# Optimization experiments

Hardware: AMD Instinct MI355X
Metric: run time of the kernel (lower is better)

## Reference

```python
import jax, jax.numpy as jnp
import numpy as np

INPUT_DIM = 1024
HIDDEN_DIM = 1024


def setup_inputs() -> dict:
    key = jax.random.key(0)
    ks = jax.random.split(key, 7)
    s = 1.0 / np.sqrt(INPUT_DIM)
    x = jax.random.normal(ks[0], (4, 2048, INPUT_DIM), dtype=jnp.float32)
    Wq = jax.random.uniform(ks[1], (INPUT_DIM, HIDDEN_DIM), minval=-s, maxval=s, dtype=jnp.float32)
    bq = jax.random.uniform(ks[2], (HIDDEN_DIM,), minval=-s, maxval=s, dtype=jnp.float32)
    Wk = jax.random.uniform(ks[3], (INPUT_DIM, HIDDEN_DIM), minval=-s, maxval=s, dtype=jnp.float32)
    bk = jax.random.uniform(ks[4], (HIDDEN_DIM,), minval=-s, maxval=s, dtype=jnp.float32)
    Wv = jax.random.uniform(ks[5], (INPUT_DIM, HIDDEN_DIM), minval=-s, maxval=s, dtype=jnp.float32)
    bv = jax.random.uniform(ks[6], (HIDDEN_DIM,), minval=-s, maxval=s, dtype=jnp.float32)
    return {"x": x, "Wq": Wq, "bq": bq, "Wk": Wk, "bk": bk, "Wv": Wv, "bv": bv}


def reference(x, Wq, bq, Wk, bk, Wv, bv):
    # Q, K, V: [B, S, H]
    Q = jnp.einsum('bsd,dh->bsh', x, Wq) + bq
    K = jnp.einsum('bsd,dh->bsh', x, Wk) + bk
    V = jnp.einsum('bsd,dh->bsh', x, Wv) + bv
    scale = 1.0 / jnp.sqrt(jnp.array(Q.shape[-1], dtype=Q.dtype))
    scores = jnp.einsum('bqh,bkh->bqk', Q, K) * scale  # [B, S, S]
    attn = jax.nn.softmax(scores, axis=-1)
    return jnp.einsum('bqk,bkh->bqh', attn, V)
```

## Files before the change

### kernel.cpp

```cpp
#include <hip/hip_runtime.h>
#include <hip/hip_bf16.h>
#include <stdint.h>

typedef unsigned short u16;
typedef __attribute__((ext_vector_type(8))) short short8;
typedef __attribute__((ext_vector_type(4))) float floatx4;

#define BATCH 4
#define SEQ   2048
#define DIM   1024

__device__ inline u16 f2bf(float f) {
  union { float f; uint32_t u; } v; v.f = f;
  uint32_t r = v.u + 0x7fffu + ((v.u >> 16) & 1u);
  return (u16)(r >> 16);
}

__device__ inline uint32_t f2bf2(float lo, float hi) {
  __hip_bfloat162 h = __float22bfloat162_rn(float2{lo, hi});
  union { __hip_bfloat162 h; uint32_t u; } v; v.h = h;
  return v.u;
}

__device__ inline void gload_lds16(const u16* g, u16* l) {
  __builtin_amdgcn_global_load_lds((const __attribute__((address_space(1))) uint32_t*)g,
                                   (__attribute__((address_space(3))) uint32_t*)l,
                                   16, 0, 0);
}

__global__ __launch_bounds__(256) void cvt_x(const float* __restrict__ in,
                                             u16* __restrict__ out,
                                             float* __restrict__ lsum) {
  size_t i = ((size_t)blockIdx.x * 256 + threadIdx.x) * 4;
  float4 v = *(const float4*)(in + i);
  uint2 o;
  o.x = f2bf2(v.x, v.y);
  o.y = f2bf2(v.z, v.w);
  *(uint2*)(out + i) = o;
  if (blockIdx.x < 8) {
    float4 z = {0.f, 0.f, 0.f, 0.f};
    *(float4*)(lsum + (size_t)blockIdx.x * 1024 + threadIdx.x * 4) = z;
  }
}

__global__ __launch_bounds__(256) void transpose_w(const float* __restrict__ Wq,
                                                   const float* __restrict__ Wk,
                                                   const float* __restrict__ Wv,
                                                   const float* __restrict__ bq,
                                                   const float* __restrict__ bk,
                                                   const float* __restrict__ bv,
                                                   u16* __restrict__ out,
                                                   float* __restrict__ bias) {
  const float* W = (blockIdx.z == 0) ? Wq : (blockIdx.z == 1) ? Wk : Wv;
  u16* o = out + (size_t)blockIdx.z * (1u << 20);
  if (blockIdx.x == 0 && blockIdx.y == 0) {
    const float* bsrc = (blockIdx.z == 0) ? bq : (blockIdx.z == 1) ? bk : bv;
    float4 b4 = *(const float4*)(bsrc + threadIdx.x * 4);
    *(float4*)(bias + blockIdx.z * 1024 + threadIdx.x * 4) = b4;
  }
  __shared__ u16 tile[32][33];
  int c0 = blockIdx.x * 32, r0 = blockIdx.y * 32;
  int tx = threadIdx.x & 31, ty = threadIdx.x >> 5;
#pragma unroll
  for (int p = 0; p < 4; ++p)
    tile[p * 8 + ty][tx] = f2bf(W[(size_t)(r0 + p * 8 + ty) * DIM + c0 + tx]);
  __syncthreads();
#pragma unroll
  for (int p = 0; p < 4; ++p)
    o[(size_t)(c0 + p * 8 + ty) * DIM + r0 + tx] = tile[tx][p * 8 + ty];
}

template <int EPI, int SWIZ, int TM>
__global__ __launch_bounds__(256, (TM == 256) ? 2 : 3)
void gemm_bt(const u16* __restrict__ A, const u16* __restrict__ Bt,
             void* __restrict__ Cv, const float* __restrict__ bias,
             float* __restrict__ lsum, int M, int N, int K,
             size_t sA, size_t sB, size_t sC) {
  constexpr int MI = TM / 32;
  constexpr int AS = TM / 64;
  __shared__ u16 ldsA[TM * 64];
  __shared__ u16 ldsB[128 * 64];
  const int lane = threadIdx.x & 63;
  const int wave = threadIdx.x >> 6;

  int mt, nt;
  if (SWIZ == 0) {
    mt = blockIdx.x; nt = blockIdx.y;
  } else if (SWIZ == 1) {
    const int lin = blockIdx.x;
    const int c = lin & 7, j = lin >> 3;
    mt = 4 * (c & 3) + (j & 3);
    nt = 8 * (c >> 2) + (j >> 2);
  } else if (SWIZ == 2) {
    const int lin = blockIdx.x;
    const int c = lin & 7, j = lin >> 3;
    mt = 4 * (c >> 1) + (j & 3);
    nt = 4 * (c & 1) + (j >> 2);
  } else if (SWIZ == 3) {
    nt = blockIdx.x; mt = blockIdx.y;
  } else {
    const int lin = blockIdx.x;
    const int c = lin & 7, j = lin >> 3;
    mt = 4 * (c & 1) + (j & 3);
    nt = 4 * (c >> 1) + (j >> 2);
  }

  const u16* Ab = A + sA * blockIdx.z + (size_t)mt * TM * K;
  const u16* Bb = Bt + sB * blockIdx.z + (size_t)nt * 128 * K;

  const int sr = lane >> 2;
  const int sc = (lane & 3) * 8;
  const u16* gA0 = Ab + (size_t)(wave * (TM / 4) + sr) * K + sc;
  const u16* gB0 = Bb + (size_t)(wave * 32 + sr) * K + sc;
  u16* lA0 = ldsA + wave * (TM / 4) * 32;
  u16* lB0 = ldsB + wave * 1024;
  constexpr int SLA = TM * 32;
  constexpr int SLB = 4096;

  const int wm = (wave >> 1) * (TM / 2);
  const int wn = (wave & 1) * 64;
  const int fr = lane & 15;
  const int fk = (lane >> 4) * 8;
  const u16* la = ldsA + (wm + fr) * 32 + fk;
  const u16* lb = ldsB + (wn + fr) * 32 + fk;

  floatx4 acc[MI][4] = {};

  for (int kt = 0; kt < K; kt += 64) {
    __syncthreads();
#pragma unroll
    for (int i = 0; i < AS; ++i) {
      gload_lds16(gA0 + kt + (size_t)(16 * i) * K, lA0 + i * 512);
      gload_lds16(gA0 + kt + 32 + (size_t)(16 * i) * K, lA0 + SLA + i * 512);
    }
#pragma unroll
    for (int i = 0; i < 2; ++i) {
      gload_lds16(gB0 + kt + (size_t)(16 * i) * K, lB0 + i * 512);
      gload_lds16(gB0 + kt + 32 + (size_t)(16 * i) * K, lB0 + SLB + i * 512);
    }
    __syncthreads();
#pragma unroll
    for (int ks = 0; ks < 2; ++ks) {
      short8 a[MI], b[4];
#pragma unroll
      for (int i = 0; i < MI; ++i)
        a[i] = *(const short8*)(la + ks * SLA + i * 512);
#pragma unroll
      for (int i = 0; i < 4; ++i)
        b[i] = *(const short8*)(lb + ks * SLB + i * 512);
#pragma unroll
      for (int mi = 0; mi < MI; ++mi)
#pragma unroll
        for (int ni = 0; ni < 4; ++ni)
          acc[mi][ni] = __builtin_amdgcn_mfma_f32_16x16x32_bf16(a[mi], b[ni], acc[mi][ni], 0, 0, 0);
    }
  }

  const int er = (lane >> 4) * 4;
  const int ec = lane & 15;
  const int r0 = mt * TM + wm;
  const int c0 = nt * 128 + wn;

  if (EPI == 0) {
    u16* C = (u16*)Cv + sC * blockIdx.z;
    const float* bz = bias + blockIdx.z * 1024;
    const float zs = (blockIdx.z == 0) ? 0.03125f : 1.0f;
#pragma unroll
    for (int mi = 0; mi < MI; ++mi)
#pragma unroll
      for (int ni = 0; ni < 4; ++ni) {
        const int col = c0 + ni * 16 + ec;
        const float bb = bz[col];
        const int row = r0 + mi * 16 + er;
        const uint32_t p0 = f2bf2((acc[mi][ni][0] + bb) * zs, (acc[mi][ni][1] + bb) * zs);
        const uint32_t p1 = f2bf2((acc[mi][ni][2] + bb) * zs, (acc[mi][ni][3] + bb) * zs);
        C[(size_t)(row + 0) * N + col] = (u16)p0;
        C[(size_t)(row + 1) * N + col] = (u16)(p0 >> 16);
        C[(size_t)(row + 2) * N + col] = (u16)p1;
        C[(size_t)(row + 3) * N + col] = (u16)(p1 >> 16);
      }
  } else if (EPI == 1) {
    u16* C = (u16*)Cv + sC * blockIdx.z;
    float* lz = lsum + blockIdx.z * 2048;
#pragma unroll
    for (int mi = 0; mi < MI; ++mi) {
      float rs[4] = {0.f, 0.f, 0.f, 0.f};
#pragma unroll
      for (int ni = 0; ni < 4; ++ni) {
        const int col = c0 + ni * 16 + ec;
        const int row = r0 + mi * 16 + er;
        float e[4];
#pragma unroll
        for (int r = 0; r < 4; ++r) {
          e[r] = exp2f(acc[mi][ni][r] * 1.44269504088896340736f);
          rs[r] += e[r];
        }
        const uint32_t p0 = f2bf2(e[0], e[1]);
        const uint32_t p1 = f2bf2(e[2], e[3]);
        C[(size_t)(row + 0) * N + col] = (u16)p0;
        C[(size_t)(row + 1) * N + col] = (u16)(p0 >> 16);
        C[(size_t)(row + 2) * N + col] = (u16)p1;
        C[(size_t)(row + 3) * N + col] = (u16)(p1 >> 16);
      }
#pragma unroll
      for (int o = 1; o < 16; o <<= 1)
#pragma unroll
        for (int r = 0; r < 4; ++r) rs[r] += __shfl_xor(rs[r], o);
      if ((lane & 15) == 0) {
#pragma unroll
        for (int r = 0; r < 4; ++r)
          atomicAdd(&lz[r0 + mi * 16 + er + r], rs[r]);
      }
    }
  } else if (EPI == 2) {
    float* C = (float*)Cv + sC * blockIdx.z;
    const float* lz = lsum + blockIdx.z * 2048;
#pragma unroll
    for (int mi = 0; mi < MI; ++mi) {
      float inv[4];
#pragma unroll
      for (int r = 0; r < 4; ++r) inv[r] = 1.0f / lz[r0 + mi * 16 + er + r];
#pragma unroll
      for (int ni = 0; ni < 4; ++ni) {
        const int col = c0 + ni * 16 + ec;
#pragma unroll
        for (int r = 0; r < 4; ++r) {
          const int row = r0 + mi * 16 + er + r;
          C[(size_t)row * N + col] = acc[mi][ni][r] * inv[r];
        }
      }
    }
  } else {
    u16* C = (u16*)Cv;
    const float* bz = bias + 2 * 1024;
#pragma unroll
    for (int mi = 0; mi < MI; ++mi) {
      float bb[4];
#pragma unroll
      for (int r = 0; r < 4; ++r) bb[r] = bz[r0 + mi * 16 + er + r];
#pragma unroll
      for (int ni = 0; ni < 4; ++ni) {
        const int col = c0 + ni * 16 + ec;
        const size_t base = (size_t)(col >> 11) * (1u << 21) + (col & 2047);
        const int row = r0 + mi * 16 + er;
        const uint32_t p0 = f2bf2(acc[mi][ni][0] + bb[0], acc[mi][ni][1] + bb[1]);
        const uint32_t p1 = f2bf2(acc[mi][ni][2] + bb[2], acc[mi][ni][3] + bb[3]);
        C[base + (size_t)(row + 0) * 2048] = (u16)p0;
        C[base + (size_t)(row + 1) * 2048] = (u16)(p0 >> 16);
        C[base + (size_t)(row + 2) * 2048] = (u16)p1;
        C[base + (size_t)(row + 3) * 2048] = (u16)(p1 >> 16);
      }
    }
  }
}

extern "C" void kernel_launch(void* const* d_in, const int* in_sizes, int n_in,
                              void* d_out, int out_size, void* d_ws, size_t ws_size,
                              hipStream_t stream) {
  const float* x  = (const float*)d_in[0];
  const float* Wq = (const float*)d_in[1];
  const float* bq = (const float*)d_in[2];
  const float* Wk = (const float*)d_in[3];
  const float* bk = (const float*)d_in[4];
  const float* Wv = (const float*)d_in[5];
  const float* bv = (const float*)d_in[6];
  float* out = (float*)d_out;

  char* ws = (char*)d_ws;
  const size_t MB = 1ull << 20;
  u16* Q    = (u16*)(ws + 0 * MB);
  u16* Kb   = (u16*)(ws + 16 * MB);
  u16* Vt   = (u16*)(ws + 48 * MB);
  u16* Xb   = (u16*)(ws + 64 * MB);
  u16* Wt   = (u16*)(ws + 80 * MB);
  float* bias = (float*)(ws + 86 * MB);
  float* lsum = (float*)(ws + 87 * MB);
  u16* P    = (u16*)(ws + 88 * MB);
  (void)Kb; (void)ws_size; (void)in_sizes; (void)n_in; (void)out_size;

  cvt_x<<<8192, 256, 0, stream>>>(x, Xb, lsum);
  transpose_w<<<dim3(32, 32, 3), 256, 0, stream>>>(Wq, Wk, Wv, bq, bk, bv, Wt, bias);
  gemm_bt<0, 0, 256><<<dim3(32, 8, 2), 256, 0, stream>>>(
      Xb, Wt, Q, bias, nullptr, 8192, 1024, 1024,
      (size_t)0, (size_t)(1u << 20), (size_t)(8u << 20));
  gemm_bt<3, 3, 128><<<dim3(64, 8, 1), 256, 0, stream>>>(
      Wt + 2 * (1u << 20), Xb, Vt, bias, nullptr, 1024, 8192, 1024,
      (size_t)0, (size_t)0, (size_t)0);
  gemm_bt<1, 4, 256><<<dim3(128, 1, 4), 256, 0, stream>>>(
      Q, Kb, P, nullptr, lsum, 2048, 2048, 1024,
      (size_t)2097152, (size_t)2097152, (size_t)4194304);
  gemm_bt<2, 2, 128><<<dim3(128, 1, 4), 256, 0, stream>>>(
      P, Vt, out, nullptr, lsum, 2048, 1024, 2048,
      (size_t)4194304, (size_t)2097152, (size_t)2097152);
}
```

Baseline: 238.0 us.

## Merge prep kernels and fuse Q/K/V projections into one launch

The x-conversion and weight-transpose kernels become a single prep kernel that dispatches on block index. The Q/K projection (256-row tiles) and the V projection (transposed output) are folded into one qkv_fused kernel with 128x128 tiles and a z dimension of 3. This removes two kernel launches and lets the V GEMM overlap with the Q/K GEMMs in one grid. In exchange, Q/K now use smaller tiles, which means more global reloads per output, and the V epilogue keeps its scattered transposed stores.

```diff
diff --git a/kernel.cpp b/kernel.cpp
--- a/kernel.cpp
+++ b/kernel.cpp
@@ -28,38 +28,44 @@
                                    16, 0, 0);
 }
 
-__global__ __launch_bounds__(256) void cvt_x(const float* __restrict__ in,
-                                             u16* __restrict__ out,
-                                             float* __restrict__ lsum) {
-  size_t i = ((size_t)blockIdx.x * 256 + threadIdx.x) * 4;
-  float4 v = *(const float4*)(in + i);
-  uint2 o;
-  o.x = f2bf2(v.x, v.y);
-  o.y = f2bf2(v.z, v.w);
-  *(uint2*)(out + i) = o;
-  if (blockIdx.x < 8) {
-    float4 z = {0.f, 0.f, 0.f, 0.f};
-    *(float4*)(lsum + (size_t)blockIdx.x * 1024 + threadIdx.x * 4) = z;
-  }
-}
-
-__global__ __launch_bounds__(256) void transpose_w(const float* __restrict__ Wq,
-                                                   const float* __restrict__ Wk,
-                                                   const float* __restrict__ Wv,
-                                                   const float* __restrict__ bq,
-                                                   const float* __restrict__ bk,
-                                                   const float* __restrict__ bv,
-                                                   u16* __restrict__ out,
-                                                   float* __restrict__ bias) {
-  const float* W = (blockIdx.z == 0) ? Wq : (blockIdx.z == 1) ? Wk : Wv;
-  u16* o = out + (size_t)blockIdx.z * (1u << 20);
-  if (blockIdx.x == 0 && blockIdx.y == 0) {
-    const float* bsrc = (blockIdx.z == 0) ? bq : (blockIdx.z == 1) ? bk : bv;
+__global__ __launch_bounds__(256) void prep(const float* __restrict__ x,
+                                            const float* __restrict__ Wq,
+                                            const float* __restrict__ Wk,
+                                            const float* __restrict__ Wv,
+                                            const float* __restrict__ bq,
+                                            const float* __restrict__ bk,
+                                            const float* __restrict__ bv,
+                                            u16* __restrict__ Xb,
+                                            u16* __restrict__ Wt,
+                                            float* __restrict__ bias,
+                                            float* __restrict__ lsum) {
+  __shared__ u16 tile[32][33];
+  const int bx = blockIdx.x;
+  if (bx < 8192) {
+    size_t i = ((size_t)bx * 256 + threadIdx.x) * 4;
+    float4 v = *(const float4*)(x + i);
+    uint2 o;
+    o.x = f2bf2(v.x, v.y);
+    o.y = f2bf2(v.z, v.w);
+    *(uint2*)(Xb + i) = o;
+    if (bx < 8) {
+      float4 z = {0.f, 0.f, 0.f, 0.f};
+      *(float4*)(lsum + (size_t)bx * 1024 + threadIdx.x * 4) = z;
+    }
+    return;
+  }
+  const int t = bx - 8192;
+  const int tz = t >> 10;
+  const int bxx = t & 31;
+  const int byy = (t >> 5) & 31;
+  const float* W = (tz == 0) ? Wq : (tz == 1) ? Wk : Wv;
+  u16* o = Wt + (size_t)tz * (1u << 20);
+  if (bxx == 0 && byy == 0) {
+    const float* bsrc = (tz == 0) ? bq : (tz == 1) ? bk : bv;
     float4 b4 = *(const float4*)(bsrc + threadIdx.x * 4);
-    *(float4*)(bias + blockIdx.z * 1024 + threadIdx.x * 4) = b4;
-  }
-  __shared__ u16 tile[32][33];
-  int c0 = blockIdx.x * 32, r0 = blockIdx.y * 32;
+    *(float4*)(bias + tz * 1024 + threadIdx.x * 4) = b4;
+  }
+  int c0 = bxx * 32, r0 = byy * 32;
   int tx = threadIdx.x & 31, ty = threadIdx.x >> 5;
 #pragma unroll
   for (int p = 0; p < 4; ++p)
@@ -70,86 +76,65 @@
     o[(size_t)(c0 + p * 8 + ty) * DIM + r0 + tx] = tile[tx][p * 8 + ty];
 }
 
-template <int EPI, int SWIZ, int TM>
-__global__ __launch_bounds__(256, (TM == 256) ? 2 : 3)
-void gemm_bt(const u16* __restrict__ A, const u16* __restrict__ Bt,
-             void* __restrict__ Cv, const float* __restrict__ bias,
-             float* __restrict__ lsum, int M, int N, int K,
-             size_t sA, size_t sB, size_t sC) {
-  constexpr int MI = TM / 32;
-  constexpr int AS = TM / 64;
-  __shared__ u16 ldsA[TM * 64];
+__global__ __launch_bounds__(256, 3)
+void qkv_fused(const u16* __restrict__ Xb, const u16* __restrict__ Wt,
+               u16* __restrict__ Q, u16* __restrict__ Vt,
+               const float* __restrict__ bias) {
+  constexpr int K = 1024;
+  __shared__ u16 ldsA[128 * 64];
   __shared__ u16 ldsB[128 * 64];
   const int lane = threadIdx.x & 63;
   const int wave = threadIdx.x >> 6;
-
-  int mt, nt;
-  if (SWIZ == 0) {
-    mt = blockIdx.x; nt = blockIdx.y;
-  } else if (SWIZ == 1) {
-    const int lin = blockIdx.x;
-    const int c = lin & 7, j = lin >> 3;
-    mt = 4 * (c & 3) + (j & 3);
-    nt = 8 * (c >> 2) + (j >> 2);
-  } else if (SWIZ == 2) {
-    const int lin = blockIdx.x;
-    const int c = lin & 7, j = lin >> 3;
-    mt = 4 * (c >> 1) + (j & 3);
-    nt = 4 * (c & 1) + (j >> 2);
-  } else if (SWIZ == 3) {
-    nt = blockIdx.x; mt = blockIdx.y;
+  const int z = blockIdx.z;
+
+  int mt, nt, N;
+  const u16 *Ab, *Bb;
+  if (z < 2) {
+    mt = blockIdx.x; nt = blockIdx.y; N = 1024;
+    Ab = Xb + (size_t)mt * 128 * K;
+    Bb = Wt + (size_t)z * (1u << 20) + (size_t)nt * 128 * K;
   } else {
-    const int lin = blockIdx.x;
-    const int c = lin & 7, j = lin >> 3;
-    mt = 4 * (c & 1) + (j & 3);
-    nt = 4 * (c >> 1) + (j >> 2);
-  }
-
-  const u16* Ab = A + sA * blockIdx.z + (size_t)mt * TM * K;
-  const u16* Bb = Bt + sB * blockIdx.z + (size_t)nt * 128 * K;
+    nt = blockIdx.x; mt = blockIdx.y; N = 8192;
+    Ab = Wt + (size_t)2 * (1u << 20) + (size_t)mt * 128 * K;
+    Bb = Xb + (size_t)nt * 128 * K;
+  }
 
   const int sr = lane >> 2;
   const int sc = (lane & 3) * 8;
-  const u16* gA0 = Ab + (size_t)(wave * (TM / 4) + sr) * K + sc;
+  const u16* gA0 = Ab + (size_t)(wave * 32 + sr) * K + sc;
   const u16* gB0 = Bb + (size_t)(wave * 32 + sr) * K + sc;
-  u16* lA0 = ldsA + wave * (TM / 4) * 32;
+  u16* lA0 = ldsA + wave * 1024;
   u16* lB0 = ldsB + wave * 1024;
-  constexpr int SLA = TM * 32;
-  constexpr int SLB = 4096;
-
-  const int wm = (wave >> 1) * (TM / 2);
+  constexpr int SL = 4096;
+
+  const int wm = (wave >> 1) * 64;
   const int wn = (wave & 1) * 64;
   const int fr = lane & 15;
   const int fk = (lane >> 4) * 8;
   const u16* la = ldsA + (wm + fr) * 32 + fk;
   const u16* lb = ldsB + (wn + fr) * 32 + fk;
 
-  floatx4 acc[MI][4] = {};
+  floatx4 acc[4][4] = {};
 
   for (int kt = 0; kt < K; kt += 64) {
     __syncthreads();
 #pragma unroll
-    for (int i = 0; i < AS; ++i) {
+    for (int i = 0; i < 2; ++i) {
       gload_lds16(gA0 + kt + (size_t)(16 * i) * K, lA0 + i * 512);
-      gload_lds16(gA0 + kt + 32 + (size_t)(16 * i) * K, lA0 + SLA + i * 512);
-    }
-#pragma unroll
-    for (int i = 0; i < 2; ++i) {
+      gload_lds16(gA0 + kt + 32 + (size_t)(16 * i) * K, lA0 + SL + i * 512);
       gload_lds16(gB0 + kt + (size_t)(16 * i) * K, lB0 + i * 512);
-      gload_lds16(gB0 + kt + 32 + (size_t)(16 * i) * K, lB0 + SLB + i * 512);
+      gload_lds16(gB0 + kt + 32 + (size_t)(16 * i) * K, lB0 + SL + i * 512);
     }
     __syncthreads();
 #pragma unroll
     for (int ks = 0; ks < 2; ++ks) {
-      short8 a[MI], b[4];
-#pragma unroll
-      for (int i = 0; i < MI; ++i)
-        a[i] = *(const short8*)(la + ks * SLA + i * 512);
-#pragma unroll
-      for (int i = 0; i < 4; ++i)
-        b[i] = *(const short8*)(lb + ks * SLB + i * 512);
-#pragma unroll
-      for (int mi = 0; mi < MI; ++mi)
+      short8 a[4], b[4];
+#pragma unroll
+      for (int i = 0; i < 4; ++i) a[i] = *(const short8*)(la + ks * SL + i * 512);
+#pragma unroll
+      for (int i = 0; i < 4; ++i) b[i] = *(const short8*)(lb + ks * SL + i * 512);
+#pragma unroll
+      for (int mi = 0; mi < 4; ++mi)
 #pragma unroll
         for (int ni = 0; ni < 4; ++ni)
           acc[mi][ni] = __builtin_amdgcn_mfma_f32_16x16x32_bf16(a[mi], b[ni], acc[mi][ni], 0, 0, 0);
@@ -158,15 +143,15 @@
 
   const int er = (lane >> 4) * 4;
   const int ec = lane & 15;
-  const int r0 = mt * TM + wm;
+  const int r0 = mt * 128 + wm;
   const int c0 = nt * 128 + wn;
 
-  if (EPI == 0) {
-    u16* C = (u16*)Cv + sC * blockIdx.z;
-    const float* bz = bias + blockIdx.z * 1024;
-    const float zs = (blockIdx.z == 0) ? 0.03125f : 1.0f;
-#pragma unroll
-    for (int mi = 0; mi < MI; ++mi)
+  if (z < 2) {
+    u16* C = Q + (size_t)z * (8u << 20);
+    const float* bz = bias + z * 1024;
+    const float zs = (z == 0) ? 0.03125f : 1.0f;
+#pragma unroll
+    for (int mi = 0; mi < 4; ++mi)
 #pragma unroll
       for (int ni = 0; ni < 4; ++ni) {
         const int col = c0 + ni * 16 + ec;
@@ -179,7 +164,111 @@
         C[(size_t)(row + 2) * N + col] = (u16)p1;
         C[(size_t)(row + 3) * N + col] = (u16)(p1 >> 16);
       }
-  } else if (EPI == 1) {
+  } else {
+    const float* bz = bias + 2 * 1024;
+#pragma unroll
+    for (int mi = 0; mi < 4; ++mi) {
+      float bb[4];
+#pragma unroll
+      for (int r = 0; r < 4; ++r) bb[r] = bz[r0 + mi * 16 + er + r];
+#pragma unroll
+      for (int ni = 0; ni < 4; ++ni) {
+        const int col = c0 + ni * 16 + ec;
+        const size_t base = (size_t)(col >> 11) * (1u << 21) + (col & 2047);
+        const int row = r0 + mi * 16 + er;
+        const uint32_t p0 = f2bf2(acc[mi][ni][0] + bb[0], acc[mi][ni][1] + bb[1]);
+        const uint32_t p1 = f2bf2(acc[mi][ni][2] + bb[2], acc[mi][ni][3] + bb[3]);
+        Vt[base + (size_t)(row + 0) * 2048] = (u16)p0;
+        Vt[base + (size_t)(row + 1) * 2048] = (u16)(p0 >> 16);
+        Vt[base + (size_t)(row + 2) * 2048] = (u16)p1;
+        Vt[base + (size_t)(row + 3) * 2048] = (u16)(p1 >> 16);
+      }
+    }
+  }
+}
+
+template <int EPI, int SWIZ, int TM>
+__global__ __launch_bounds__(256, (TM == 256) ? 2 : 3)
+void gemm_bt(const u16* __restrict__ A, const u16* __restrict__ Bt,
+             void* __restrict__ Cv, float* __restrict__ lsum,
+             int M, int N, int K, size_t sA, size_t sB, size_t sC) {
+  constexpr int MI = TM / 32;
+  constexpr int AS = TM / 64;
+  __shared__ u16 ldsA[TM * 64];
+  __shared__ u16 ldsB[128 * 64];
+  const int lane = threadIdx.x & 63;
+  const int wave = threadIdx.x >> 6;
+
+  int mt, nt;
+  if (SWIZ == 2) {
+    const int lin = blockIdx.x;
+    const int c = lin & 7, j = lin >> 3;
+    mt = 4 * (c >> 1) + (j & 3);
+    nt = 4 * (c & 1) + (j >> 2);
+  } else {
+    const int lin = blockIdx.x;
+    const int c = lin & 7, j = lin >> 3;
+    mt = 4 * (c & 1) + (j & 3);
+    nt = 4 * (c >> 1) + (j >> 2);
+  }
+
+  const u16* Ab = A + sA * blockIdx.z + (size_t)mt * TM * K;
+  const u16* Bb = Bt + sB * blockIdx.z + (size_t)nt * 128 * K;
+
+  const int sr = lane >> 2;
+  const int sc = (lane & 3) * 8;
+  const u16* gA0 = Ab + (size_t)(wave * (TM / 4) + sr) * K + sc;
+  const u16* gB0 = Bb + (size_t)(wave * 32 + sr) * K + sc;
+  u16* lA0 = ldsA + wave * (TM / 4) * 32;
+  u16* lB0 = ldsB + wave * 1024;
+  constexpr int SLA = TM * 32;
+  constexpr int SLB = 4096;
+
+  const int wm = (wave >> 1) * (TM / 2);
+  const int wn = (wave & 1) * 64;
+  const int fr = lane & 15;
+  const int fk = (lane >> 4) * 8;
+  const u16* la = ldsA + (wm + fr) * 32 + fk;
+  const u16* lb = ldsB + (wn + fr) * 32 + fk;
+
+  floatx4 acc[MI][4] = {};
+
+  for (int kt = 0; kt < K; kt += 64) {
+    __syncthreads();
+#pragma unroll
+    for (int i = 0; i < AS; ++i) {
+      gload_lds16(gA0 + kt + (size_t)(16 * i) * K, lA0 + i * 512);
+      gload_lds16(gA0 + kt + 32 + (size_t)(16 * i) * K, lA0 + SLA + i * 512);
+    }
+#pragma unroll
+    for (int i = 0; i < 2; ++i) {
+      gload_lds16(gB0 + kt + (size_t)(16 * i) * K, lB0 + i * 512);
+      gload_lds16(gB0 + kt + 32 + (size_t)(16 * i) * K, lB0 + SLB + i * 512);
+    }
+    __syncthreads();
+#pragma unroll
+    for (int ks = 0; ks < 2; ++ks) {
+      short8 a[MI], b[4];
+#pragma unroll
+      for (int i = 0; i < MI; ++i)
+        a[i] = *(const short8*)(la + ks * SLA + i * 512);
+#pragma unroll
+      for (int i = 0; i < 4; ++i)
+        b[i] = *(const short8*)(lb + ks * SLB + i * 512);
+#pragma unroll
+      for (int mi = 0; mi < MI; ++mi)
+#pragma unroll
+        for (int ni = 0; ni < 4; ++ni)
+          acc[mi][ni] = __builtin_amdgcn_mfma_f32_16x16x32_bf16(a[mi], b[ni], acc[mi][ni], 0, 0, 0);
+    }
+  }
+
+  const int er = (lane >> 4) * 4;
+  const int ec = lane & 15;
+  const int r0 = mt * TM + wm;
+  const int c0 = nt * 128 + wn;
+
+  if (EPI == 1) {
     u16* C = (u16*)Cv + sC * blockIdx.z;
     float* lz = lsum + blockIdx.z * 2048;
 #pragma unroll
@@ -212,7 +301,7 @@
           atomicAdd(&lz[r0 + mi * 16 + er + r], rs[r]);
       }
     }
-  } else if (EPI == 2) {
+  } else {
     float* C = (float*)Cv + sC * blockIdx.z;
     const float* lz = lsum + blockIdx.z * 2048;
 #pragma unroll
@@ -228,27 +317,6 @@
           const int row = r0 + mi * 16 + er + r;
           C[(size_t)row * N + col] = acc[mi][ni][r] * inv[r];
         }
-      }
-    }
-  } else {
-    u16* C = (u16*)Cv;
-    const float* bz = bias + 2 * 1024;
-#pragma unroll
-    for (int mi = 0; mi < MI; ++mi) {
-      float bb[4];
-#pragma unroll
-      for (int r = 0; r < 4; ++r) bb[r] = bz[r0 + mi * 16 + er + r];
-#pragma unroll
-      for (int ni = 0; ni < 4; ++ni) {
-        const int col = c0 + ni * 16 + ec;
-        const size_t base = (size_t)(col >> 11) * (1u << 21) + (col & 2047);
-        const int row = r0 + mi * 16 + er;
-        const uint32_t p0 = f2bf2(acc[mi][ni][0] + bb[0], acc[mi][ni][1] + bb[1]);
-        const uint32_t p1 = f2bf2(acc[mi][ni][2] + bb[2], acc[mi][ni][3] + bb[3]);
-        C[base + (size_t)(row + 0) * 2048] = (u16)p0;
-        C[base + (size_t)(row + 1) * 2048] = (u16)(p0 >> 16);
-        C[base + (size_t)(row + 2) * 2048] = (u16)p1;
-        C[base + (size_t)(row + 3) * 2048] = (u16)(p1 >> 16);
       }
     }
   }
@@ -278,18 +346,12 @@
   u16* P    = (u16*)(ws + 88 * MB);
   (void)Kb; (void)ws_size; (void)in_sizes; (void)n_in; (void)out_size;
 
-  cvt_x<<<8192, 256, 0, stream>>>(x, Xb, lsum);
-  transpose_w<<<dim3(32, 32, 3), 256, 0, stream>>>(Wq, Wk, Wv, bq, bk, bv, Wt, bias);
-  gemm_bt<0, 0, 256><<<dim3(32, 8, 2), 256, 0, stream>>>(
-      Xb, Wt, Q, bias, nullptr, 8192, 1024, 1024,
-      (size_t)0, (size_t)(1u << 20), (size_t)(8u << 20));
-  gemm_bt<3, 3, 128><<<dim3(64, 8, 1), 256, 0, stream>>>(
-      Wt + 2 * (1u << 20), Xb, Vt, bias, nullptr, 1024, 8192, 1024,
-      (size_t)0, (size_t)0, (size_t)0);
+  prep<<<11264, 256, 0, stream>>>(x, Wq, Wk, Wv, bq, bk, bv, Xb, Wt, bias, lsum);
+  qkv_fused<<<dim3(64, 8, 3), 256, 0, stream>>>(Xb, Wt, Q, Vt, bias);
   gemm_bt<1, 4, 256><<<dim3(128, 1, 4), 256, 0, stream>>>(
-      Q, Kb, P, nullptr, lsum, 2048, 2048, 1024,
+      Q, Kb, P, lsum, 2048, 2048, 1024,
       (size_t)2097152, (size_t)2097152, (size_t)4194304);
   gemm_bt<2, 2, 128><<<dim3(128, 1, 4), 256, 0, stream>>>(
-      P, Vt, out, nullptr, lsum, 2048, 1024, 2048,
+      P, Vt, out, lsum, 2048, 1024, 2048,
       (size_t)4194304, (size_t)2097152, (size_t)2097152);
 }
```

Result: no change. 234.9 us (-1.3%).
